# Kernel tuning notes

Measured on AMD Instinct MI355X. Metric: run time of the kernel, lower is better.

## Reference

```python
import jax, jax.numpy as jnp
import numpy as np

B, NQ, NK = 2, 2048, 2048
QD, CD, H, DH = 1024, 768, 16, 64
INNER = H * DH


def setup_inputs() -> dict:
    key = jax.random.key(0)
    ks = jax.random.split(key, 8)
    x = jax.random.normal(ks[0], (B, NQ, QD), jnp.float32)
    context = jax.random.normal(ks[1], (B, NK, CD), jnp.float32)
    mask = jax.random.randint(ks[2], (B, 1, NQ, NK), 0, 2) > 0
    s = lambda d: 1.0 / np.sqrt(d)
    Wq = jax.random.normal(ks[3], (INNER, QD), jnp.float32) * s(QD)
    Wk = jax.random.normal(ks[4], (INNER, CD), jnp.float32) * s(CD)
    Wv = jax.random.normal(ks[5], (INNER, CD), jnp.float32) * s(CD)
    Wo = jax.random.normal(ks[6], (QD, INNER), jnp.float32) * s(INNER)
    bo = jax.random.normal(ks[7], (QD,), jnp.float32) * 0.01
    return {"x": x, "context": context, "mask": mask,
            "Wq": Wq, "Wk": Wk, "Wv": Wv, "Wo": Wo, "bo": bo}


def reference(x, context, mask, Wq, Wk, Wv, Wo, bo):
    scale = DH ** -0.5
    # QKV projections (Linear, no bias): [b, n, inner] -> [b, n, h, d]
    q = (x @ Wq.T).reshape(B, NQ, H, DH)
    k = (context @ Wk.T).reshape(B, NK, H, DH)
    v = (context @ Wv.T).reshape(B, NK, H, DH)
    # additive bias built from boolean mask (masked_fill with -finfo.max/2)
    max_neg = -jnp.finfo(q.dtype).max / 2
    bias = jnp.where(mask, jnp.zeros((), q.dtype), max_neg)  # [b,1,nq,nk]
    scores = jnp.einsum('bqhd,bkhd->bhqk', q, k) * scale + bias
    attn = jax.nn.softmax(scores, axis=-1)
    out = jnp.einsum('bhqk,bkhd->bqhd', attn, v).reshape(B, NQ, INNER)
    return out @ Wo.T + bo
```

## Files before the change

kernel.cpp:

```cpp
#include <hip/hip_runtime.h>
#include <float.h>
#include <stdint.h>

#define C_B     2
#define C_NQ    2048
#define C_NK    2048
#define C_QD    1024
#define C_CD    768
#define C_H     16
#define C_DH    64
#define C_INNER 1024

typedef __bf16 bf16;
typedef __attribute__((ext_vector_type(8))) __bf16 bf16x8;
typedef __attribute__((ext_vector_type(4))) __bf16 bf16x4;
typedef __attribute__((ext_vector_type(4))) float f32x4;
typedef __attribute__((ext_vector_type(16))) float f32x16;

#if __has_builtin(__builtin_amdgcn_exp2f)
#define EXP2(x) __builtin_amdgcn_exp2f(x)
#else
#define EXP2(x) __expf((x) * 0.69314718056f)
#endif

__device__ __forceinline__ void async_copy16(const bf16* g, bf16* l) {
  __builtin_amdgcn_global_load_lds(
      (const __attribute__((address_space(1))) void*)g,
      (__attribute__((address_space(3))) void*)l,
      16, 0, 0);
}

__global__ __launch_bounds__(256) void prep(const float* __restrict__ s0, const float* __restrict__ s1,
                                            const float* __restrict__ s2, const float* __restrict__ s3,
                                            const float* __restrict__ s4, const float* __restrict__ s5,
                                            bf16* __restrict__ d0, bf16* __restrict__ d1,
                                            bf16* __restrict__ d2, bf16* __restrict__ d3,
                                            bf16* __restrict__ d4, bf16* __restrict__ d5,
                                            const int* __restrict__ mask,
                                            unsigned long long* __restrict__ mb) {
  const int stride = gridDim.x * blockDim.x;
  for (int idx = blockIdx.x * blockDim.x + threadIdx.x; idx < 2752512; idx += stride) {
    const float* src; bf16* dst; int loc;
    if      (idx < 1048576) { src = s0; dst = d0; loc = idx; }
    else if (idx < 1835008) { src = s1; dst = d1; loc = idx - 1048576; }
    else if (idx < 2097152) { src = s2; dst = d2; loc = idx - 1835008; }
    else if (idx < 2293760) { src = s3; dst = d3; loc = idx - 2097152; }
    else if (idx < 2490368) { src = s4; dst = d4; loc = idx - 2293760; }
    else                    { src = s5; dst = d5; loc = idx - 2490368; }
    float4 f = *(const float4*)&src[loc * 4];
    bf16x4 o = { (bf16)f.x, (bf16)f.y, (bf16)f.z, (bf16)f.w };
    *(bf16x4*)&dst[loc * 4] = o;
  }
  const int lane = threadIdx.x & 63;
  const int wid  = (blockIdx.x * blockDim.x + threadIdx.x) >> 6;
  const int nw   = (gridDim.x * blockDim.x) >> 6;
  for (int w = wid; w < 131072; w += nw) {
    int v = mask[(size_t)w * 64 + lane];
    unsigned long long bb = __ballot(v != 0);
    if (lane == 0) mb[w] = bb;
  }
}

__device__ __forceinline__ void gemm_core(const bf16* __restrict__ A,
                                          const bf16* __restrict__ W,
                                          int m0, int n0, int K,
                                          bf16* As0, bf16* As1, bf16* Bs0, bf16* Bs1,
                                          f32x4 (&acc)[4][4],
                                          int w, int lane) {
  const int l15 = lane & 15, lg = lane >> 4;
  const int wm = w >> 1, wn = w & 1;
  bf16* AsA[2] = {As0, As1};
  bf16* BsA[2] = {Bs0, Bs1};

  auto stage = [&](int nb, int k0) {
#pragma unroll
    for (int i = 0; i < 2; ++i) {
      const int chunk = w * 128 + i * 64 + lane;
      const int row = chunk >> 2;
      const int srcb = ((chunk & 3) ^ (row & 3)) * 8;
      async_copy16(A + (size_t)(m0 + row) * K + k0 + srcb, &AsA[nb][chunk * 8]);
      async_copy16(W + (size_t)(n0 + row) * K + k0 + srcb, &BsA[nb][chunk * 8]);
    }
  };

  stage(0, 0);
  int cur = 0;
  for (int k0 = 0; k0 < K; k0 += 32) {
    __syncthreads();
    if (k0 + 32 < K) stage(cur ^ 1, k0 + 32);

    bf16x8 af[4], bfv[4];
#pragma unroll
    for (int mi = 0; mi < 4; ++mi) {
      const int row = wm * 64 + mi * 16 + l15;
      af[mi] = *(const bf16x8*)&AsA[cur][row * 32 + ((lg ^ (row & 3)) * 8)];
    }
#pragma unroll
    for (int ni = 0; ni < 4; ++ni) {
      const int row = wn * 64 + ni * 16 + l15;
      bfv[ni] = *(const bf16x8*)&BsA[cur][row * 32 + ((lg ^ (row & 3)) * 8)];
    }
#pragma unroll
    for (int mi = 0; mi < 4; ++mi)
#pragma unroll
      for (int ni = 0; ni < 4; ++ni)
        acc[mi][ni] = __builtin_amdgcn_mfma_f32_16x16x32_bf16(af[mi], bfv[ni],
                                                              acc[mi][ni], 0, 0, 0);
    cur ^= 1;
  }
}

__global__ __launch_bounds__(256) void gemm_qkv(const bf16* __restrict__ xb,
                                                const bf16* __restrict__ wqb,
                                                bf16* __restrict__ Qb,
                                                const bf16* __restrict__ cb,
                                                const bf16* __restrict__ wkv,
                                                bf16* __restrict__ Kb,
                                                bf16* __restrict__ Vb,
                                                float qscale) {
  __shared__ __align__(16) bf16 As[2][128 * 32];
  __shared__ __align__(16) bf16 Bs[2][128 * 32];

  const int bid = blockIdx.x;
  const int t = threadIdx.x, w = t >> 6, lane = t & 63;
  const int l15 = lane & 15, lg = lane >> 4;
  const int wm = w >> 1, wn = w & 1;

  const bf16 *A, *W;
  int m0, n0, K, N;
  float oscale;
  if (bid < 256) {
    A = xb; W = wqb; n0 = (bid & 7) * 128; m0 = (bid >> 3) * 128;
    K = C_QD; N = C_INNER; oscale = qscale;
  } else {
    const int b2 = bid - 256;
    A = cb; W = wkv; n0 = (b2 & 15) * 128; m0 = (b2 >> 4) * 128;
    K = C_CD; N = 2 * C_INNER; oscale = 1.0f;
  }

  f32x4 acc[4][4] = {};
  gemm_core(A, W, m0, n0, K, As[0], As[1], Bs[0], Bs[1], acc, w, lane);

#pragma unroll
  for (int mi = 0; mi < 4; ++mi)
#pragma unroll
    for (int ni = 0; ni < 4; ++ni)
#pragma unroll
      for (int r = 0; r < 4; ++r) {
        const int row = m0 + wm * 64 + mi * 16 + lg * 4 + r;
        const int col = n0 + wn * 64 + ni * 16 + l15;
        const float v = acc[mi][ni][r] * oscale;
        bf16* dst; int cc;
        if (bid < 256)            { dst = Qb; cc = col; }
        else if (col < C_INNER)   { dst = Kb; cc = col; }
        else                      { dst = Vb; cc = col - C_INNER; }
        dst[(size_t)row * C_INNER + cc] = (bf16)v;
      }
}

__global__ __launch_bounds__(256) void gemm_out(const bf16* __restrict__ A,
                                                const bf16* __restrict__ W,
                                                const float* __restrict__ bias,
                                                float* __restrict__ Cout,
                                                int M, int N, int K) {
  __shared__ __align__(16) bf16 As[2][128 * 32];
  __shared__ __align__(16) bf16 Bs[2][128 * 32];
  const int t = threadIdx.x, w = t >> 6, lane = t & 63;
  const int l15 = lane & 15, lg = lane >> 4;
  const int wm = w >> 1, wn = w & 1;
  const int m0 = blockIdx.y * 128, n0 = blockIdx.x * 128;

  f32x4 acc[4][4] = {};
  gemm_core(A, W, m0, n0, K, As[0], As[1], Bs[0], Bs[1], acc, w, lane);

#pragma unroll
  for (int mi = 0; mi < 4; ++mi)
#pragma unroll
    for (int ni = 0; ni < 4; ++ni)
#pragma unroll
      for (int r = 0; r < 4; ++r) {
        const int row = m0 + wm * 64 + mi * 16 + lg * 4 + r;
        const int col = n0 + wn * 64 + ni * 16 + l15;
        Cout[(size_t)row * N + col] = acc[mi][ni][r] + bias[col];
      }
}

__global__ __launch_bounds__(256) void vtrans(const bf16* __restrict__ V,
                                              bf16* __restrict__ Vt) {
  __shared__ __align__(16) bf16 T[64][80];
  const int kt = blockIdx.x, h = blockIdx.y, b = blockIdx.z;
  const int t = threadIdx.x;
  {
    const int kl = t >> 2, db = (t & 3) * 16;
    const bf16* src = &V[((size_t)(b * C_NK + kt * 64 + kl)) * C_INNER + h * 64 + db];
    *(bf16x8*)&T[kl][db]     = *(const bf16x8*)&src[0];
    *(bf16x8*)&T[kl][db + 8] = *(const bf16x8*)&src[8];
  }
  __syncthreads();
  {
    const int d = t >> 2, kb = (t & 3) * 16;
    const int P0[8] = {0, 1, 2, 3, 8, 9, 10, 11};
    const int P1[8] = {4, 5, 6, 7, 12, 13, 14, 15};
    bf16x8 o0, o1;
#pragma unroll
    for (int j = 0; j < 8; ++j) { o0[j] = T[kb + P0[j]][d]; o1[j] = T[kb + P1[j]][d]; }
    bf16* dst = &Vt[((size_t)((b * C_H + h) * C_DH + d)) * C_NK + kt * 64 + kb];
    *(bf16x8*)&dst[0] = o0;
    *(bf16x8*)&dst[8] = o1;
  }
}

__global__ __launch_bounds__(256, 4) void attn_fwd(const bf16* __restrict__ Q,
                                                   const bf16* __restrict__ K,
                                                   const bf16* __restrict__ Vt,
                                                   const unsigned long long* __restrict__ MB,
                                                   bf16* __restrict__ O0,
                                                   bf16* __restrict__ O1,
                                                   float2* __restrict__ LM) {
  __shared__ __align__(16) bf16 Ks[2][64 * 64];
  __shared__ __align__(16) bf16 Vs[2][64 * 64];

  const int bid = blockIdx.x;
  const int swz = ((bid & 7) << 7) | (bid >> 3);
  const int qt = swz & 15, h = (swz >> 4) & 15, zz = swz >> 8;
  const int half = zz >> 1, b = zz & 1;
  const int t = threadIdx.x, wq = t >> 6, lane = t & 63;
  const int l31 = lane & 31, hi = lane >> 5;
  const int q = qt * 128 + wq * 32 + l31;

  bf16x8 qf[4];
  {
    const bf16* qp = Q + ((size_t)(b * C_NQ + q)) * C_INNER + h * C_DH;
#pragma unroll
    for (int db = 0; db < 4; ++db)
      qf[db] = *(const bf16x8*)&qp[db * 16 + hi * 8];
  }

  float m_run = -3.0e38f, l_run = 0.f;
  f32x16 acc_o[2] = {};

  auto stage = [&](int nb, int ktA) {
#pragma unroll
    for (int i = 0; i < 2; ++i) {
      const int chunk = wq * 128 + i * 64 + lane;
      const int row = chunk >> 3, pcb = chunk & 7;
      const int srcb = (pcb ^ (row & 7)) * 8;
      const bf16* kg = K + ((size_t)(b * C_NK + ktA * 64 + row)) * C_INNER + h * C_DH + srcb;
      async_copy16(kg, &Ks[nb][chunk * 8]);
      const bf16* vg = Vt + ((size_t)((b * C_H + h) * C_DH + row)) * C_NK + ktA * 64 + srcb;
      async_copy16(vg, &Vs[nb][chunk * 8]);
    }
  };

  const int kt0 = half * 16;
  stage(0, kt0);
  int cur = 0;

  for (int i = 0; i < 16; ++i) {
    const int ktA = kt0 + i;
    const unsigned long long wd =
        MB[((size_t)(b * C_NQ + q)) * (C_NK / 64) + ktA] >> (hi * 4);
    const unsigned mlo = (unsigned)wd, mhi = (unsigned)(wd >> 32);

    __syncthreads();
    if (i + 1 < 16) stage(cur ^ 1, ktA + 1);

    f32x16 s[2] = {};
    __builtin_amdgcn_s_setprio(1);
#pragma unroll
    for (int kb = 0; kb < 2; ++kb)
#pragma unroll
      for (int db = 0; db < 4; ++db) {
        const int row = kb * 32 + l31;
        const int cb = (db * 2 + hi) ^ (row & 7);
        bf16x8 kf = *(const bf16x8*)&Ks[cur][row * 64 + cb * 8];
        s[kb] = __builtin_amdgcn_mfma_f32_32x32x16_bf16(kf, qf[db], s[kb], 0, 0, 0);
      }
    __builtin_amdgcn_s_setprio(0);

    float pm = -1.0e30f;
#pragma unroll
    for (int kb = 0; kb < 2; ++kb)
#pragma unroll
      for (int reg = 0; reg < 16; ++reg) pm = fmaxf(pm, s[kb][reg]);
    pm = fmaxf(pm, __shfl_xor(pm, 32));

    if (!__all(pm <= m_run + 8.0f)) {
      const float mn = fmaxf(m_run, pm);
      const float f = EXP2(m_run - mn);
      m_run = mn;
      l_run *= f;
#pragma unroll
      for (int d2 = 0; d2 < 2; ++d2)
#pragma unroll
        for (int reg = 0; reg < 16; ++reg)
          acc_o[d2][reg] *= f;
    }

    bf16x8 pfr[4];
    float ps = 0.f;
#pragma unroll
    for (int kb = 0; kb < 2; ++kb) {
      const unsigned mw = kb ? mhi : mlo;
#pragma unroll
      for (int kss = 0; kss < 2; ++kss) {
        bf16x8 pf;
#pragma unroll
        for (int j = 0; j < 8; ++j) {
          const int reg = kss * 8 + j;
          const int pos = (reg & 3) + 8 * (reg >> 2);
          float p = EXP2(s[kb][reg] - m_run);
          p = ((mw >> pos) & 1u) ? p : 0.f;
          ps += p;
          pf[j] = (bf16)p;
        }
        pfr[kb * 2 + kss] = pf;
      }
    }
    l_run += ps;

    __builtin_amdgcn_s_setprio(1);
#pragma unroll
    for (int ks = 0; ks < 4; ++ks) {
#pragma unroll
      for (int d2 = 0; d2 < 2; ++d2) {
        const int row = d2 * 32 + l31;
        const int cb = (ks * 2 + hi) ^ (row & 7);
        bf16x8 vf = *(const bf16x8*)&Vs[cur][row * 64 + cb * 8];
        acc_o[d2] = __builtin_amdgcn_mfma_f32_32x32x16_bf16(vf, pfr[ks], acc_o[d2], 0, 0, 0);
      }
    }
    __builtin_amdgcn_s_setprio(0);
    cur ^= 1;
  }

  {
    const float l_tot = l_run + __shfl_xor(l_run, 32);
    const size_t row = (size_t)(b * C_H + h) * C_NQ + q;
    bf16* op = (half ? O1 : O0) + row * 64;
#pragma unroll
    for (int d2 = 0; d2 < 2; ++d2)
#pragma unroll
      for (int bb = 0; bb < 4; ++bb) {
        bf16x4 o;
#pragma unroll
        for (int rr = 0; rr < 4; ++rr)
          o[rr] = (bf16)(acc_o[d2][bb * 4 + rr]);
        *(bf16x4*)&op[d2 * 32 + bb * 8 + hi * 4] = o;
      }
    if (hi == 0) LM[(size_t)half * 65536 + row] = make_float2(m_run, l_tot);
  }
}

__global__ __launch_bounds__(256) void merge_halves(const bf16* __restrict__ O0,
                                                    const bf16* __restrict__ O1,
                                                    const float2* __restrict__ LM,
                                                    bf16* __restrict__ AO) {
  const int t = threadIdx.x;
  const int r = blockIdx.x * 32 + (t >> 3);
  const int dc = (t & 7) * 8;
  const float2 lm0 = LM[r], lm1 = LM[65536 + r];
  const float ms = fmaxf(lm0.x, lm1.x);
  const float w0 = EXP2(lm0.x - ms), w1 = EXP2(lm1.x - ms);
  const float denom = lm0.y * w0 + lm1.y * w1;
  const float s0 = w0 / denom, s1 = w1 / denom;
  bf16x8 a = *(const bf16x8*)&O0[(size_t)r * 64 + dc];
  bf16x8 c = *(const bf16x8*)&O1[(size_t)r * 64 + dc];
  bf16x8 o;
#pragma unroll
  for (int j = 0; j < 8; ++j)
    o[j] = (bf16)((float)a[j] * s0 + (float)c[j] * s1);
  const int q = r & 2047, bh = r >> 11, hh = bh & 15, bb = bh >> 4;
  *(bf16x8*)&AO[((size_t)(bb * C_NQ + q)) * C_INNER + hh * 64 + dc] = o;
}

extern "C" void kernel_launch(void* const* d_in, const int* in_sizes, int n_in,
                              void* d_out, int out_size, void* d_ws, size_t ws_size,
                              hipStream_t stream) {
  const float* x   = (const float*)d_in[0];
  const float* ctx = (const float*)d_in[1];
  const int*   msk = (const int*)d_in[2];
  const float* Wq  = (const float*)d_in[3];
  const float* Wk  = (const float*)d_in[4];
  const float* Wv  = (const float*)d_in[5];
  const float* Wo  = (const float*)d_in[6];
  const float* bo  = (const float*)d_in[7];
  float* out = (float*)d_out;

  bf16* ws  = (bf16*)d_ws;
  bf16* xb  = ws;
  bf16* cb  = xb  + 4194304;
  bf16* wqb = cb  + 3145728;
  bf16* wkb = wqb + 1048576;
  bf16* wvb = wkb + 786432;
  bf16* wob = wvb + 786432;
  bf16* Qb  = wob + 1048576;
  bf16* Kb  = Qb  + 4194304;
  bf16* Vb  = Kb  + 4194304;
  bf16* AOb = Vb  + 4194304;
  unsigned long long* mb = (unsigned long long*)(AOb + 4194304);
  float2* lm = (float2*)(mb + 131072);
  bf16* Vtb = xb;
  bf16* O0  = cb;
  bf16* O1  = Vb;

  dim3 blk(256);
  prep<<<2048, blk, 0, stream>>>(x, ctx, Wq, Wk, Wv, Wo,
                                 xb, cb, wqb, wkb, wvb, wob, msk, mb);

  const float qscale = 0.125f * 1.44269504f;
  gemm_qkv<<<768, blk, 0, stream>>>(xb, wqb, Qb, cb, wkb, Kb, Vb, qscale);

  vtrans<<<dim3(C_NK / 64, C_H, C_B), blk, 0, stream>>>(Vb, Vtb);

  attn_fwd<<<1024, blk, 0, stream>>>(Qb, Kb, Vtb, mb, O0, O1, lm);

  merge_halves<<<2048, blk, 0, stream>>>(O0, O1, lm, AOb);

  const int MQ = C_B * C_NQ;
  gemm_out<<<dim3(C_QD / 128, MQ / 128), blk, 0, stream>>>(
      AOb, wob, bo, out, MQ, C_QD, C_INNER);
}
```

Before: 153.0 us.

## Split attention KV range into quarters and shrink output GEMM tiles

The attention kernel now splits the key range into four chunks instead of two, launching twice as many blocks, and a merge kernel combines the four partial results using their running max and sum. The output projection GEMM uses 64-row tiles with its own staging loop, giving more blocks for better occupancy on a GPU with many compute units. The max and sum reductions inside attention are rewritten as trees to shorten dependency chains. In exchange there is more partial-output traffic and a heavier merge, and the extra partial buffers are placed in the output buffer as scratch before it is overwritten.

```diff
diff --git a/kernel.cpp b/kernel.cpp
--- a/kernel.cpp
+++ b/kernel.cpp
@@ -127,15 +127,15 @@
   const int wm = w >> 1, wn = w & 1;
 
   const bf16 *A, *W;
-  int m0, n0, K, N;
+  int m0, n0, K;
   float oscale;
   if (bid < 256) {
     A = xb; W = wqb; n0 = (bid & 7) * 128; m0 = (bid >> 3) * 128;
-    K = C_QD; N = C_INNER; oscale = qscale;
+    K = C_QD; oscale = qscale;
   } else {
     const int b2 = bid - 256;
     A = cb; W = wkv; n0 = (b2 & 15) * 128; m0 = (b2 >> 4) * 128;
-    K = C_CD; N = 2 * C_INNER; oscale = 1.0f;
+    K = C_CD; oscale = 1.0f;
   }
 
   f32x4 acc[4][4] = {};
@@ -163,23 +163,64 @@
                                                 const float* __restrict__ bias,
                                                 float* __restrict__ Cout,
                                                 int M, int N, int K) {
-  __shared__ __align__(16) bf16 As[2][128 * 32];
+  __shared__ __align__(16) bf16 As[2][64 * 32];
   __shared__ __align__(16) bf16 Bs[2][128 * 32];
   const int t = threadIdx.x, w = t >> 6, lane = t & 63;
   const int l15 = lane & 15, lg = lane >> 4;
   const int wm = w >> 1, wn = w & 1;
-  const int m0 = blockIdx.y * 128, n0 = blockIdx.x * 128;
-
-  f32x4 acc[4][4] = {};
-  gemm_core(A, W, m0, n0, K, As[0], As[1], Bs[0], Bs[1], acc, w, lane);
-
-#pragma unroll
-  for (int mi = 0; mi < 4; ++mi)
+  const int m0 = blockIdx.y * 64, n0 = blockIdx.x * 128;
+
+  f32x4 acc[2][4] = {};
+
+  auto stage = [&](int nb, int k0) {
+    {
+      const int ca = w * 64 + lane;
+      const int arow = ca >> 2;
+      const int asrc = ((ca & 3) ^ (arow & 3)) * 8;
+      async_copy16(A + (size_t)(m0 + arow) * K + k0 + asrc, &As[nb][ca * 8]);
+    }
+#pragma unroll
+    for (int i = 0; i < 2; ++i) {
+      const int cbk = w * 128 + i * 64 + lane;
+      const int brow = cbk >> 2;
+      const int bsrc = ((cbk & 3) ^ (brow & 3)) * 8;
+      async_copy16(W + (size_t)(n0 + brow) * K + k0 + bsrc, &Bs[nb][cbk * 8]);
+    }
+  };
+
+  stage(0, 0);
+  int cur = 0;
+  for (int k0 = 0; k0 < K; k0 += 32) {
+    __syncthreads();
+    if (k0 + 32 < K) stage(cur ^ 1, k0 + 32);
+
+    bf16x8 af[2], bfv[4];
+#pragma unroll
+    for (int mi = 0; mi < 2; ++mi) {
+      const int row = wm * 32 + mi * 16 + l15;
+      af[mi] = *(const bf16x8*)&As[cur][row * 32 + ((lg ^ (row & 3)) * 8)];
+    }
+#pragma unroll
+    for (int ni = 0; ni < 4; ++ni) {
+      const int row = wn * 64 + ni * 16 + l15;
+      bfv[ni] = *(const bf16x8*)&Bs[cur][row * 32 + ((lg ^ (row & 3)) * 8)];
+    }
+#pragma unroll
+    for (int mi = 0; mi < 2; ++mi)
+#pragma unroll
+      for (int ni = 0; ni < 4; ++ni)
+        acc[mi][ni] = __builtin_amdgcn_mfma_f32_16x16x32_bf16(af[mi], bfv[ni],
+                                                              acc[mi][ni], 0, 0, 0);
+    cur ^= 1;
+  }
+
+#pragma unroll
+  for (int mi = 0; mi < 2; ++mi)
 #pragma unroll
     for (int ni = 0; ni < 4; ++ni)
 #pragma unroll
       for (int r = 0; r < 4; ++r) {
-        const int row = m0 + wm * 64 + mi * 16 + lg * 4 + r;
+        const int row = m0 + wm * 32 + mi * 16 + lg * 4 + r;
         const int col = n0 + wn * 64 + ni * 16 + l15;
         Cout[(size_t)row * N + col] = acc[mi][ni][r] + bias[col];
       }
@@ -216,14 +257,16 @@
                                                    const unsigned long long* __restrict__ MB,
                                                    bf16* __restrict__ O0,
                                                    bf16* __restrict__ O1,
+                                                   bf16* __restrict__ O2,
+                                                   bf16* __restrict__ O3,
                                                    float2* __restrict__ LM) {
   __shared__ __align__(16) bf16 Ks[2][64 * 64];
   __shared__ __align__(16) bf16 Vs[2][64 * 64];
 
   const int bid = blockIdx.x;
-  const int swz = ((bid & 7) << 7) | (bid >> 3);
+  const int swz = ((bid & 7) << 8) | (bid >> 3);
   const int qt = swz & 15, h = (swz >> 4) & 15, zz = swz >> 8;
-  const int half = zz >> 1, b = zz & 1;
+  const int quarter = zz >> 1, b = zz & 1;
   const int t = threadIdx.x, wq = t >> 6, lane = t & 63;
   const int l31 = lane & 31, hi = lane >> 5;
   const int q = qt * 128 + wq * 32 + l31;
@@ -252,18 +295,18 @@
     }
   };
 
-  const int kt0 = half * 16;
+  const int kt0 = quarter * 8;
   stage(0, kt0);
   int cur = 0;
 
-  for (int i = 0; i < 16; ++i) {
+  for (int i = 0; i < 8; ++i) {
     const int ktA = kt0 + i;
     const unsigned long long wd =
         MB[((size_t)(b * C_NQ + q)) * (C_NK / 64) + ktA] >> (hi * 4);
     const unsigned mlo = (unsigned)wd, mhi = (unsigned)(wd >> 32);
 
     __syncthreads();
-    if (i + 1 < 16) stage(cur ^ 1, ktA + 1);
+    if (i + 1 < 8) stage(cur ^ 1, ktA + 1);
 
     f32x16 s[2] = {};
     __builtin_amdgcn_s_setprio(1);
@@ -278,11 +321,19 @@
       }
     __builtin_amdgcn_s_setprio(0);
 
-    float pm = -1.0e30f;
-#pragma unroll
-    for (int kb = 0; kb < 2; ++kb)
-#pragma unroll
-      for (int reg = 0; reg < 16; ++reg) pm = fmaxf(pm, s[kb][reg]);
+    float pm;
+    {
+      float t16[16];
+#pragma unroll
+      for (int r = 0; r < 16; ++r) t16[r] = fmaxf(s[0][r], s[1][r]);
+      float t8[8];
+#pragma unroll
+      for (int r = 0; r < 8; ++r) t8[r] = fmaxf(t16[r], t16[r + 8]);
+      float t4[4];
+#pragma unroll
+      for (int r = 0; r < 4; ++r) t4[r] = fmaxf(t8[r], t8[r + 4]);
+      pm = fmaxf(fmaxf(t4[0], t4[1]), fmaxf(t4[2], t4[3]));
+    }
     pm = fmaxf(pm, __shfl_xor(pm, 32));
 
     if (!__all(pm <= m_run + 8.0f)) {
@@ -298,26 +349,29 @@
     }
 
     bf16x8 pfr[4];
-    float ps = 0.f;
+    float psb[4];
 #pragma unroll
     for (int kb = 0; kb < 2; ++kb) {
       const unsigned mw = kb ? mhi : mlo;
 #pragma unroll
       for (int kss = 0; kss < 2; ++kss) {
         bf16x8 pf;
+        float pv[8];
 #pragma unroll
         for (int j = 0; j < 8; ++j) {
           const int reg = kss * 8 + j;
           const int pos = (reg & 3) + 8 * (reg >> 2);
           float p = EXP2(s[kb][reg] - m_run);
           p = ((mw >> pos) & 1u) ? p : 0.f;
-          ps += p;
+          pv[j] = p;
           pf[j] = (bf16)p;
         }
+        psb[kb * 2 + kss] = ((pv[0] + pv[1]) + (pv[2] + pv[3])) +
+                            ((pv[4] + pv[5]) + (pv[6] + pv[7]));
         pfr[kb * 2 + kss] = pf;
       }
     }
-    l_run += ps;
+    l_run += (psb[0] + psb[1]) + (psb[2] + psb[3]);
 
     __builtin_amdgcn_s_setprio(1);
 #pragma unroll
@@ -337,7 +391,8 @@
   {
     const float l_tot = l_run + __shfl_xor(l_run, 32);
     const size_t row = (size_t)(b * C_H + h) * C_NQ + q;
-    bf16* op = (half ? O1 : O0) + row * 64;
+    bf16* op = (quarter == 0) ? O0 : (quarter == 1) ? O1 : (quarter == 2) ? O2 : O3;
+    op += row * 64;
 #pragma unroll
     for (int d2 = 0; d2 < 2; ++d2)
 #pragma unroll
@@ -348,28 +403,36 @@
           o[rr] = (bf16)(acc_o[d2][bb * 4 + rr]);
         *(bf16x4*)&op[d2 * 32 + bb * 8 + hi * 4] = o;
       }
-    if (hi == 0) LM[(size_t)half * 65536 + row] = make_float2(m_run, l_tot);
-  }
-}
-
-__global__ __launch_bounds__(256) void merge_halves(const bf16* __restrict__ O0,
-                                                    const bf16* __restrict__ O1,
-                                                    const float2* __restrict__ LM,
-                                                    bf16* __restrict__ AO) {
+    if (hi == 0) LM[(size_t)quarter * 65536 + row] = make_float2(m_run, l_tot);
+  }
+}
+
+__global__ __launch_bounds__(256) void merge_quarters(const bf16* __restrict__ O0,
+                                                      const bf16* __restrict__ O1,
+                                                      const bf16* __restrict__ O2,
+                                                      const bf16* __restrict__ O3,
+                                                      const float2* __restrict__ LM,
+                                                      bf16* __restrict__ AO) {
   const int t = threadIdx.x;
   const int r = blockIdx.x * 32 + (t >> 3);
   const int dc = (t & 7) * 8;
   const float2 lm0 = LM[r], lm1 = LM[65536 + r];
-  const float ms = fmaxf(lm0.x, lm1.x);
+  const float2 lm2 = LM[131072 + r], lm3 = LM[196608 + r];
+  const float ms = fmaxf(fmaxf(lm0.x, lm1.x), fmaxf(lm2.x, lm3.x));
   const float w0 = EXP2(lm0.x - ms), w1 = EXP2(lm1.x - ms);
-  const float denom = lm0.y * w0 + lm1.y * w1;
-  const float s0 = w0 / denom, s1 = w1 / denom;
+  const float w2 = EXP2(lm2.x - ms), w3 = EXP2(lm3.x - ms);
+  const float denom = (lm0.y * w0 + lm1.y * w1) + (lm2.y * w2 + lm3.y * w3);
+  const float inv = 1.0f / denom;
+  const float s0 = w0 * inv, s1 = w1 * inv, s2 = w2 * inv, s3 = w3 * inv;
   bf16x8 a = *(const bf16x8*)&O0[(size_t)r * 64 + dc];
   bf16x8 c = *(const bf16x8*)&O1[(size_t)r * 64 + dc];
+  bf16x8 e = *(const bf16x8*)&O2[(size_t)r * 64 + dc];
+  bf16x8 g = *(const bf16x8*)&O3[(size_t)r * 64 + dc];
   bf16x8 o;
 #pragma unroll
   for (int j = 0; j < 8; ++j)
-    o[j] = (bf16)((float)a[j] * s0 + (float)c[j] * s1);
+    o[j] = (bf16)(((float)a[j] * s0 + (float)c[j] * s1) +
+                  ((float)e[j] * s2 + (float)g[j] * s3));
   const int q = r & 2047, bh = r >> 11, hh = bh & 15, bb = bh >> 4;
   *(bf16x8*)&AO[((size_t)(bb * C_NQ + q)) * C_INNER + hh * 64 + dc] = o;
 }
@@ -403,6 +466,8 @@
   bf16* Vtb = xb;
   bf16* O0  = cb;
   bf16* O1  = Vb;
+  bf16* O2  = (bf16*)d_out;
+  bf16* O3  = O2 + 4194304;
 
   dim3 blk(256);
   prep<<<2048, blk, 0, stream>>>(x, ctx, Wq, Wk, Wv, Wo,
@@ -413,11 +478,11 @@
 
   vtrans<<<dim3(C_NK / 64, C_H, C_B), blk, 0, stream>>>(Vb, Vtb);
 
-  attn_fwd<<<1024, blk, 0, stream>>>(Qb, Kb, Vtb, mb, O0, O1, lm);
-
-  merge_halves<<<2048, blk, 0, stream>>>(O0, O1, lm, AOb);
+  attn_fwd<<<2048, blk, 0, stream>>>(Qb, Kb, Vtb, mb, O0, O1, O2, O3, lm);
+
+  merge_quarters<<<2048, blk, 0, stream>>>(O0, O1, O2, O3, lm, AOb);
 
   const int MQ = C_B * C_NQ;
-  gemm_out<<<dim3(C_QD / 128, MQ / 128), blk, 0, stream>>>(
+  gemm_out<<<dim3(C_QD / 128, MQ / 64), blk, 0, stream>>>(
       AOb, wob, bo, out, MQ, C_QD, C_INNER);
 }
```

New measurement: 174.4 us. 14.0% more time.
